# Performance work log

Hardware: AMD Instinct MI355X
Metric: run time of the kernel (lower is better)

## Reference

```python
import jax, jax.numpy as jnp
import numpy as np

_CORNER_T = jnp.array([[0.5, 0.5], [-0.5, 0.5], [-0.5, -0.5], [0.5, -0.5]], dtype=jnp.float32)

def _cross2(a, b):
    return a[..., 0] * b[..., 1] - a[..., 1] * b[..., 0]

def _corners(b):
    # b: (7,) box (x, y, z, dx, dy, dz, heading) -> (4, 2) BEV corners
    local = _CORNER_T * jnp.stack([b[3], b[4]])  # (4,2)
    c, s = jnp.cos(b[6]), jnp.sin(b[6])
    x = local[:, 0] * c - local[:, 1] * s + b[0]
    y = local[:, 0] * s + local[:, 1] * c + b[1]
    return jnp.stack([x, y], axis=-1)

def _pts_in_box(pts, b):
    # pts: (...,2); rotate into the box frame and test half-extents
    d = pts - b[:2]
    c, s = jnp.cos(b[6]), jnp.sin(b[6])
    qx = d[..., 0] * c + d[..., 1] * s
    qy = -d[..., 0] * s + d[..., 1] * c
    return (jnp.abs(qx) <= b[3] * 0.5 + 1e-5) & (jnp.abs(qy) <= b[4] * 0.5 + 1e-5)

def _pair_bev_inter(box_a, box_b):
    # Intersection area of two rotated BEV rectangles (convex polygon, <=8 verts).
    ca, cb = _corners(box_a), _corners(box_b)  # (4,2) each
    p1, p2 = ca, jnp.roll(ca, -1, axis=0)
    q1, q2 = cb, jnp.roll(cb, -1, axis=0)
    d1 = (p2 - p1)[:, None, :]          # (4,1,2)
    d2 = (q2 - q1)[None, :, :]          # (1,4,2)
    r = q1[None, :, :] - p1[:, None, :]  # (4,4,2)
    den = _cross2(d1, d2)               # (4,4)
    safe = jnp.where(jnp.abs(den) > 1e-8, den, 1.0)
    t = _cross2(r, d2) / safe
    u = _cross2(r, d1) / safe
    iv = (jnp.abs(den) > 1e-8) & (t >= -1e-6) & (t <= 1 + 1e-6) & (u >= -1e-6) & (u <= 1 + 1e-6)
    ip = p1[:, None, :] + t[..., None] * d1  # (4,4,2) edge-edge intersections
    cand = jnp.concatenate([ca, cb, ip.reshape(16, 2)], axis=0)  # (24,2)
    valid = jnp.concatenate([_pts_in_box(ca, box_b), _pts_in_box(cb, box_a), iv.reshape(16)], axis=0)
    vf = valid.astype(cand.dtype)
    n = jnp.sum(vf)
    cen = jnp.sum(cand * vf[:, None], axis=0) / jnp.maximum(n, 1.0)
    ang = jnp.where(valid, jnp.arctan2(cand[:, 1] - cen[1], cand[:, 0] - cen[0]), 1e9)
    order = jnp.argsort(ang)  # valid points first, CCW around centroid
    pts = cand[order]
    vs = valid[order]
    pts = jnp.where(vs[:, None], pts, pts[0])  # pad with first vertex (zero area)
    area = 0.5 * jnp.abs(jnp.sum(_cross2(pts, jnp.roll(pts, -1, axis=0))))
    return jnp.where(n >= 3, area, 0.0)

def _aligned_iou3d(ba, bb):
    # ba, bb: (N,7) paired boxes -> (N,) 3D IoU (matches boxes_aligned_iou3d_gpu)
    inter_bev = jax.vmap(_pair_bev_inter)(ba, bb)
    top = jnp.minimum(ba[:, 2] + ba[:, 5] * 0.5, bb[:, 2] + bb[:, 5] * 0.5)
    bot = jnp.maximum(ba[:, 2] - ba[:, 5] * 0.5, bb[:, 2] - bb[:, 5] * 0.5)
    inter = inter_bev * jnp.maximum(top - bot, 0.0)
    va = ba[:, 3] * ba[:, 4] * ba[:, 5]
    vb = bb[:, 3] * bb[:, 4] * bb[:, 5]
    return inter / jnp.maximum(va + vb - inter, 1e-6)

def setup_inputs() -> dict:
    key = jax.random.key(0)
    ks = jax.random.split(key, 8)
    B, C, H, W, M, DIM = 16, 1, 512, 512, 500, 7
    iou_pred = jax.random.normal(ks[0], (B, C, H, W), dtype=jnp.float32)
    mask = jax.random.randint(ks[1], (B, M), 0, 2, dtype=jnp.int32)
    ind = jax.random.randint(ks[2], (B, M), 0, H * W, dtype=jnp.int32)
    # box_pred map: realistic positive dims on channels 3:6
    box_pred = jax.random.normal(ks[3], (B, DIM, H, W), dtype=jnp.float32) * 5.0
    dims = jax.random.uniform(ks[4], (B, 3, H, W), minval=1.0, maxval=5.0)
    box_pred = box_pred.at[:, 3:6].set(dims)
    # gt boxes: centers in [0,100), dims in [1,5), heading in [-pi,pi)
    ctr = jax.random.uniform(ks[5], (B, M, 3), minval=0.0, maxval=100.0)
    gdims = jax.random.uniform(ks[6], (B, M, 3), minval=1.0, maxval=5.0)
    ang = jax.random.uniform(ks[7], (B, M, 1), minval=-np.pi, maxval=np.pi)
    box_gt = jnp.concatenate([ctr, gdims, ang], axis=-1).astype(jnp.float32)
    return {"iou_pred": iou_pred, "mask": mask, "ind": ind, "box_pred": box_pred, "box_gt": box_gt}

def reference(iou_pred, mask, ind, box_pred, box_gt):
    B, C, H, W = iou_pred.shape
    M = ind.shape[1]
    D = box_pred.shape[1]
    ind = ind.astype(jnp.int32)
    # _transpose_and_gather_feat: permute BCHW->B(HW)C then gather rows by ind
    feat = iou_pred.transpose(0, 2, 3, 1).reshape(B, H * W, C)
    pred = jnp.take_along_axis(feat, ind[..., None], axis=1)[..., 0]  # (B,M)
    bfeat = box_pred.transpose(0, 2, 3, 1).reshape(B, H * W, D)
    pbox = jnp.take_along_axis(bfeat, jnp.broadcast_to(ind[..., None], (B, M, D)), axis=1)
    iou = _aligned_iou3d(pbox.reshape(-1, D), box_gt.reshape(-1, D)).reshape(B, M)
    target = jax.lax.stop_gradient(2.0 * iou - 1.0)  # CUDA IoU op carries no grad
    m = mask.astype(pred.dtype)  # boolean mask-select expressed as weighting
    loss = jnp.sum(jnp.abs(pred - target) * m) / (jnp.sum(m) + 1e-4)
    return loss
```

## Files before the change

### kernel.cpp

```cpp
#include <hip/hip_runtime.h>
#include <math.h>

namespace {
constexpr int Bc = 16;
constexpr int Mc = 500;
constexpr int Hc = 512;
constexpr int Wc = 512;
constexpr int HWc = Hc * Wc;
constexpr int Dc = 7;
constexpr int NPAIR = Bc * Mc;
constexpr int BLOCK = 256;
constexpr int NBLK = (NPAIR + BLOCK - 1) / BLOCK;
}

__device__ float bev_inter(const float* __restrict__ a, const float* __restrict__ b) {
    const float cA = cosf(a[6]), sA = sinf(a[6]);
    const float cB = cosf(b[6]), sB = sinf(b[6]);

    const float t0[4] = {0.5f, -0.5f, -0.5f, 0.5f};
    const float t1[4] = {0.5f, 0.5f, -0.5f, -0.5f};

    float cax[4], cay[4], cbx[4], cby[4];
#pragma unroll
    for (int i = 0; i < 4; ++i) {
        float lx = t0[i] * a[3], ly = t1[i] * a[4];
        cax[i] = lx * cA - ly * sA + a[0];
        cay[i] = lx * sA + ly * cA + a[1];
        lx = t0[i] * b[3]; ly = t1[i] * b[4];
        cbx[i] = lx * cB - ly * sB + b[0];
        cby[i] = lx * sB + ly * cB + b[1];
    }

    float px[24], py[24];
    int n = 0;

    const float hbx = b[3] * 0.5f + 1e-5f, hby = b[4] * 0.5f + 1e-5f;
#pragma unroll
    for (int i = 0; i < 4; ++i) {
        float dx = cax[i] - b[0], dy = cay[i] - b[1];
        float qx = dx * cB + dy * sB;
        float qy = -dx * sB + dy * cB;
        if (fabsf(qx) <= hbx && fabsf(qy) <= hby) { px[n] = cax[i]; py[n] = cay[i]; ++n; }
    }
    const float hax = a[3] * 0.5f + 1e-5f, hay = a[4] * 0.5f + 1e-5f;
#pragma unroll
    for (int i = 0; i < 4; ++i) {
        float dx = cbx[i] - a[0], dy = cby[i] - a[1];
        float qx = dx * cA + dy * sA;
        float qy = -dx * sA + dy * cA;
        if (fabsf(qx) <= hax && fabsf(qy) <= hay) { px[n] = cbx[i]; py[n] = cby[i]; ++n; }
    }
#pragma unroll
    for (int i = 0; i < 4; ++i) {
        const float p1x = cax[i], p1y = cay[i];
        const float d1x = cax[(i + 1) & 3] - p1x, d1y = cay[(i + 1) & 3] - p1y;
#pragma unroll
        for (int j = 0; j < 4; ++j) {
            const float q1x = cbx[j], q1y = cby[j];
            const float d2x = cbx[(j + 1) & 3] - q1x, d2y = cby[(j + 1) & 3] - q1y;
            const float den = d1x * d2y - d1y * d2x;
            if (fabsf(den) > 1e-8f) {
                const float rx = q1x - p1x, ry = q1y - p1y;
                const float t = (rx * d2y - ry * d2x) / den;
                const float u = (rx * d1y - ry * d1x) / den;
                if (t >= -1e-6f && t <= 1.f + 1e-6f && u >= -1e-6f && u <= 1.f + 1e-6f) {
                    px[n] = p1x + t * d1x;
                    py[n] = p1y + t * d1y;
                    ++n;
                }
            }
        }
    }

    if (n < 3) return 0.f;

    float cx = 0.f, cy = 0.f;
    for (int k = 0; k < n; ++k) { cx += px[k]; cy += py[k]; }
    const float inv_n = 1.f / (float)n;
    cx *= inv_n; cy *= inv_n;

    float ang[24];
    for (int k = 0; k < n; ++k) ang[k] = atan2f(py[k] - cy, px[k] - cx);

    for (int k = 1; k < n; ++k) {
        const float ka = ang[k], kx = px[k], ky = py[k];
        int j = k - 1;
        while (j >= 0 && ang[j] > ka) {
            ang[j + 1] = ang[j]; px[j + 1] = px[j]; py[j + 1] = py[j];
            --j;
        }
        ang[j + 1] = ka; px[j + 1] = kx; py[j + 1] = ky;
    }

    float area = 0.f;
    for (int k = 0; k < n; ++k) {
        const int k2 = (k + 1 == n) ? 0 : k + 1;
        area += px[k] * py[k2] - py[k] * px[k2];
    }
    return 0.5f * fabsf(area);
}

__device__ float iou3d(const float* __restrict__ a, const float* __restrict__ b) {
    const float inter_bev = bev_inter(a, b);
    const float top = fminf(a[2] + a[5] * 0.5f, b[2] + b[5] * 0.5f);
    const float bot = fmaxf(a[2] - a[5] * 0.5f, b[2] - b[5] * 0.5f);
    const float inter = inter_bev * fmaxf(top - bot, 0.f);
    const float va = a[3] * a[4] * a[5];
    const float vb = b[3] * b[4] * b[5];
    return inter / fmaxf(va + vb - inter, 1e-6f);
}

__global__ void __launch_bounds__(BLOCK)
iou_loss_pairs(const float* __restrict__ iou_pred,
               const int* __restrict__ mask,
               const int* __restrict__ ind,
               const float* __restrict__ box_pred,
               const float* __restrict__ box_gt,
               float* __restrict__ ws) {
    const int idx = blockIdx.x * BLOCK + threadIdx.x;
    float term = 0.f, mv = 0.f;
    if (idx < NPAIR) {
        const int b = idx / Mc;
        const int i = ind[idx];
        const float pred = iou_pred[(size_t)b * HWc + i];

        float pb[7], gb[7];
        const float* bp = box_pred + (size_t)b * Dc * HWc + i;
#pragma unroll
        for (int d = 0; d < 7; ++d) pb[d] = bp[(size_t)d * HWc];
#pragma unroll
        for (int d = 0; d < 7; ++d) gb[d] = box_gt[(size_t)idx * 7 + d];

        const float iou = iou3d(pb, gb);
        const float target = 2.f * iou - 1.f;
        const float mm = (float)mask[idx];
        term = fabsf(pred - target) * mm;
        mv = mm;
    }

#pragma unroll
    for (int off = 32; off > 0; off >>= 1) {
        term += __shfl_down(term, off);
        mv += __shfl_down(mv, off);
    }
    __shared__ float st[BLOCK / 64], sm[BLOCK / 64];
    const int wave = threadIdx.x >> 6, lane = threadIdx.x & 63;
    if (lane == 0) { st[wave] = term; sm[wave] = mv; }
    __syncthreads();
    if (threadIdx.x == 0) {
        float t = 0.f, m = 0.f;
#pragma unroll
        for (int w = 0; w < BLOCK / 64; ++w) { t += st[w]; m += sm[w]; }
        ws[blockIdx.x * 2] = t;
        ws[blockIdx.x * 2 + 1] = m;
    }
}

__global__ void iou_loss_finalize(const float* __restrict__ ws, float* __restrict__ out) {
    const int t = threadIdx.x;
    float s = (t < NBLK) ? ws[t * 2] : 0.f;
    float m = (t < NBLK) ? ws[t * 2 + 1] : 0.f;
#pragma unroll
    for (int off = 32; off > 0; off >>= 1) {
        s += __shfl_down(s, off);
        m += __shfl_down(m, off);
    }
    if (t == 0) out[0] = s / (m + 1e-4f);
}

extern "C" void kernel_launch(void* const* d_in, const int* in_sizes, int n_in,
                              void* d_out, int out_size, void* d_ws, size_t ws_size,
                              hipStream_t stream) {
    const float* iou_pred = (const float*)d_in[0];
    const int* mask = (const int*)d_in[1];
    const int* ind = (const int*)d_in[2];
    const float* box_pred = (const float*)d_in[3];
    const float* box_gt = (const float*)d_in[4];
    float* ws = (float*)d_ws;
    float* out = (float*)d_out;

    iou_loss_pairs<<<NBLK, BLOCK, 0, stream>>>(iou_pred, mask, ind, box_pred, box_gt, ws);
    iou_loss_finalize<<<1, 64, 0, stream>>>(ws, out);
}
```

Baseline: 169.0 us.

## Replace sort-based polygon intersection with Sutherland-Hodgman clipping in box frame

Computes the BEV intersection by moving box A into box B's local frame and clipping it against B's four axis-aligned half-planes (Sutherland-Hodgman), using fixed 8-entry register arrays and no atan2 or insertion sort. This removes the divergent sort, the per-point atan2 calls and the 24-entry local arrays that likely spilled to scratch memory. It also switches to the fast __sincosf intrinsic and shrinks blocks to a single wave so the shared-memory reduction disappears. The trade-offs are slightly different numerics from the loose epsilons and fast trig, and the workspace layout is hardcoded to an offset of 128, which assumes NBLK stays at or below 128 (here it is 125).

Result: faster. 161.0 us (-4.7%).

```diff
diff --git a/kernel.cpp b/kernel.cpp
--- a/kernel.cpp
+++ b/kernel.cpp
@@ -9,95 +9,89 @@
 constexpr int HWc = Hc * Wc;
 constexpr int Dc = 7;
 constexpr int NPAIR = Bc * Mc;
-constexpr int BLOCK = 256;
+constexpr int BLOCK = 64;
 constexpr int NBLK = (NPAIR + BLOCK - 1) / BLOCK;
 }
 
+__device__ __forceinline__ void push_pt(float (&qx)[8], float (&qy)[8], int& m,
+                                        float nx, float ny) {
+#pragma unroll
+    for (int s = 0; s < 8; ++s) {
+        if (s == m) { qx[s] = nx; qy[s] = ny; }
+    }
+    ++m;
+}
+
+__device__ __forceinline__ void clip_pass(float (&Px)[8], float (&Py)[8], int& n,
+                                          float sx, float sy, float lim) {
+    float Qx[8], Qy[8];
+    int m = 0;
+    const int nn = n;
+#pragma unroll
+    for (int k = 0; k < 8; ++k) {
+        if (k < nn) {
+            const float cx = Px[k], cy = Py[k];
+            float nx, ny;
+            if (k == 7) { nx = Px[0]; ny = Py[0]; }
+            else if (k + 1 == nn) { nx = Px[0]; ny = Py[0]; }
+            else { nx = Px[k + 1]; ny = Py[k + 1]; }
+            const float dc = lim - (sx * cx + sy * cy);
+            const float dn = lim - (sx * nx + sy * ny);
+            const bool cin = dc >= 0.f;
+            const bool nin = dn >= 0.f;
+            if (cin) push_pt(Qx, Qy, m, cx, cy);
+            if (cin != nin) {
+                const float t = dc / (dc - dn);
+                push_pt(Qx, Qy, m, cx + t * (nx - cx), cy + t * (ny - cy));
+            }
+        }
+    }
+    n = m;
+#pragma unroll
+    for (int k = 0; k < 8; ++k) { Px[k] = Qx[k]; Py[k] = Qy[k]; }
+}
+
 __device__ float bev_inter(const float* __restrict__ a, const float* __restrict__ b) {
-    const float cA = cosf(a[6]), sA = sinf(a[6]);
-    const float cB = cosf(b[6]), sB = sinf(b[6]);
+    float sA, cA, sB, cB;
+    __sincosf(a[6], &sA, &cA);
+    __sincosf(b[6], &sB, &cB);
+    const float cR = cA * cB + sA * sB;
+    const float sR = sA * cB - cA * sB;
+    const float dxw = a[0] - b[0], dyw = a[1] - b[1];
+    const float ox = dxw * cB + dyw * sB;
+    const float oy = -dxw * sB + dyw * cB;
 
     const float t0[4] = {0.5f, -0.5f, -0.5f, 0.5f};
     const float t1[4] = {0.5f, 0.5f, -0.5f, -0.5f};
-
-    float cax[4], cay[4], cbx[4], cby[4];
+    float Px[8], Py[8];
 #pragma unroll
     for (int i = 0; i < 4; ++i) {
-        float lx = t0[i] * a[3], ly = t1[i] * a[4];
-        cax[i] = lx * cA - ly * sA + a[0];
-        cay[i] = lx * sA + ly * cA + a[1];
-        lx = t0[i] * b[3]; ly = t1[i] * b[4];
-        cbx[i] = lx * cB - ly * sB + b[0];
-        cby[i] = lx * sB + ly * cB + b[1];
-    }
-
-    float px[24], py[24];
-    int n = 0;
-
-    const float hbx = b[3] * 0.5f + 1e-5f, hby = b[4] * 0.5f + 1e-5f;
-#pragma unroll
-    for (int i = 0; i < 4; ++i) {
-        float dx = cax[i] - b[0], dy = cay[i] - b[1];
-        float qx = dx * cB + dy * sB;
-        float qy = -dx * sB + dy * cB;
-        if (fabsf(qx) <= hbx && fabsf(qy) <= hby) { px[n] = cax[i]; py[n] = cay[i]; ++n; }
-    }
-    const float hax = a[3] * 0.5f + 1e-5f, hay = a[4] * 0.5f + 1e-5f;
-#pragma unroll
-    for (int i = 0; i < 4; ++i) {
-        float dx = cbx[i] - a[0], dy = cby[i] - a[1];
-        float qx = dx * cA + dy * sA;
-        float qy = -dx * sA + dy * cA;
-        if (fabsf(qx) <= hax && fabsf(qy) <= hay) { px[n] = cbx[i]; py[n] = cby[i]; ++n; }
+        const float lx = t0[i] * a[3], ly = t1[i] * a[4];
+        Px[i] = lx * cR - ly * sR + ox;
+        Py[i] = lx * sR + ly * cR + oy;
     }
 #pragma unroll
-    for (int i = 0; i < 4; ++i) {
-        const float p1x = cax[i], p1y = cay[i];
-        const float d1x = cax[(i + 1) & 3] - p1x, d1y = cay[(i + 1) & 3] - p1y;
+    for (int i = 4; i < 8; ++i) { Px[i] = 0.f; Py[i] = 0.f; }
+    int n = 4;
+
+    const float hx = b[3] * 0.5f, hy = b[4] * 0.5f;
+    clip_pass(Px, Py, n, 1.f, 0.f, hx);
+    clip_pass(Px, Py, n, -1.f, 0.f, hx);
+    clip_pass(Px, Py, n, 0.f, 1.f, hy);
+    clip_pass(Px, Py, n, 0.f, -1.f, hy);
+
+    float area2 = 0.f;
 #pragma unroll
-        for (int j = 0; j < 4; ++j) {
-            const float q1x = cbx[j], q1y = cby[j];
-            const float d2x = cbx[(j + 1) & 3] - q1x, d2y = cby[(j + 1) & 3] - q1y;
-            const float den = d1x * d2y - d1y * d2x;
-            if (fabsf(den) > 1e-8f) {
-                const float rx = q1x - p1x, ry = q1y - p1y;
-                const float t = (rx * d2y - ry * d2x) / den;
-                const float u = (rx * d1y - ry * d1x) / den;
-                if (t >= -1e-6f && t <= 1.f + 1e-6f && u >= -1e-6f && u <= 1.f + 1e-6f) {
-                    px[n] = p1x + t * d1x;
-                    py[n] = p1y + t * d1y;
-                    ++n;
-                }
-            }
+    for (int k = 0; k < 8; ++k) {
+        if (k < n) {
+            float nx, ny;
+            if (k == 7) { nx = Px[0]; ny = Py[0]; }
+            else if (k + 1 == n) { nx = Px[0]; ny = Py[0]; }
+            else { nx = Px[k + 1]; ny = Py[k + 1]; }
+            area2 += Px[k] * ny - Py[k] * nx;
         }
     }
-
-    if (n < 3) return 0.f;
-
-    float cx = 0.f, cy = 0.f;
-    for (int k = 0; k < n; ++k) { cx += px[k]; cy += py[k]; }
-    const float inv_n = 1.f / (float)n;
-    cx *= inv_n; cy *= inv_n;
-
-    float ang[24];
-    for (int k = 0; k < n; ++k) ang[k] = atan2f(py[k] - cy, px[k] - cx);
-
-    for (int k = 1; k < n; ++k) {
-        const float ka = ang[k], kx = px[k], ky = py[k];
-        int j = k - 1;
-        while (j >= 0 && ang[j] > ka) {
-            ang[j + 1] = ang[j]; px[j + 1] = px[j]; py[j + 1] = py[j];
-            --j;
-        }
-        ang[j + 1] = ka; px[j + 1] = kx; py[j + 1] = ky;
-    }
-
-    float area = 0.f;
-    for (int k = 0; k < n; ++k) {
-        const int k2 = (k + 1 == n) ? 0 : k + 1;
-        area += px[k] * py[k2] - py[k] * px[k2];
-    }
-    return 0.5f * fabsf(area);
+    return 0.5f * fabsf(area2);
 }
 
 __device__ float iou3d(const float* __restrict__ a, const float* __restrict__ b) {
@@ -143,23 +137,19 @@
         term += __shfl_down(term, off);
         mv += __shfl_down(mv, off);
     }
-    __shared__ float st[BLOCK / 64], sm[BLOCK / 64];
-    const int wave = threadIdx.x >> 6, lane = threadIdx.x & 63;
-    if (lane == 0) { st[wave] = term; sm[wave] = mv; }
-    __syncthreads();
     if (threadIdx.x == 0) {
-        float t = 0.f, m = 0.f;
-#pragma unroll
-        for (int w = 0; w < BLOCK / 64; ++w) { t += st[w]; m += sm[w]; }
-        ws[blockIdx.x * 2] = t;
-        ws[blockIdx.x * 2 + 1] = m;
+        ws[blockIdx.x] = term;
+        ws[128 + blockIdx.x] = mv;
     }
 }
 
 __global__ void iou_loss_finalize(const float* __restrict__ ws, float* __restrict__ out) {
     const int t = threadIdx.x;
-    float s = (t < NBLK) ? ws[t * 2] : 0.f;
-    float m = (t < NBLK) ? ws[t * 2 + 1] : 0.f;
+    float s = 0.f, m = 0.f;
+    for (int i = t; i < NBLK; i += 64) {
+        s += ws[i];
+        m += ws[128 + i];
+    }
 #pragma unroll
     for (int off = 32; off > 0; off >>= 1) {
         s += __shfl_down(s, off);
```
